# Optimization experiments

Hardware: AMD Instinct MI355X
Metric: run time of the kernel (lower is better)

## Reference

```python
import jax, jax.numpy as jnp
import numpy as np

INPUT_SIZE = 128
OUTPUT_SIZE = 128
HIDDEN = 8
BATCH = 1024
N = INPUT_SIZE * OUTPUT_SIZE  # number of tiny subnetworks


def setup_inputs() -> dict:
    key = jax.random.key(0)
    ks = jax.random.split(key, 7)
    s = 0.5  # modest init scale
    return {
        "x": jax.random.normal(ks[0], (BATCH, INPUT_SIZE), dtype=jnp.float32),
        "W1": jax.random.normal(ks[1], (N, HIDDEN, 1), dtype=jnp.float32) * s,
        "b1": jax.random.normal(ks[2], (N, HIDDEN), dtype=jnp.float32) * s,
        "W2": jax.random.normal(ks[3], (N, HIDDEN, HIDDEN), dtype=jnp.float32) * s,
        "b2": jax.random.normal(ks[4], (N, HIDDEN), dtype=jnp.float32) * s,
        "W3": jax.random.normal(ks[5], (N, 1, HIDDEN), dtype=jnp.float32) * s,
        "b3": jax.random.normal(ks[6], (N, 1), dtype=jnp.float32) * s,
    }


def reference(x, W1, b1, W2, b2, W3, b3):
    # x: [B, input_size]. Subnet n = i*output_size + o consumes feature i.
    B = x.shape[0]
    # x.T repeat_interleave(output_size, dim=0).unsqueeze(-1) -> [N, B, 1]
    xe = jnp.repeat(x.T, OUTPUT_SIZE, axis=0)[:, :, None]
    # torch Linear: y = x @ W.T + b, batched over subnet dim n
    h = jax.nn.relu(jnp.einsum('nbi,nhi->nbh', xe, W1) + b1[:, None, :])
    h = jax.nn.relu(jnp.einsum('nbi,nhi->nbh', h, W2) + b2[:, None, :])
    o = jnp.einsum('nbh,noh->nbo', h, W3) + b3[:, None, :]  # [N, B, 1]
    o = o[..., 0].reshape(INPUT_SIZE, OUTPUT_SIZE, B)
    return o.sum(axis=0).T  # [B, output_size]
```

## Files before the change

### kernel.cpp

```cpp
#include <hip/hip_runtime.h>

#define INPUT_SIZE 128
#define OUTPUT_SIZE 128
#define HIDDEN 8
#define BATCH 1024

#define ICH 16
#define IPC (INPUT_SIZE / ICH)
#define TPB 128
#define BPT 8
#define SLOT 68

typedef __fp16 half2v __attribute__((ext_vector_type(2)));

#if defined(__has_builtin)
#if __has_builtin(__builtin_amdgcn_fdot2)
#define HAS_FDOT2 1
#endif
#endif
#ifndef HAS_FDOT2
#define HAS_FDOT2 0
#endif

__global__ void prep_kernel(const float* __restrict__ x,
                            const float* __restrict__ W2,
                            float* __restrict__ xT,
                            __fp16* __restrict__ W2h) {
    if (blockIdx.x < 128) {
        __shared__ float tile[32][33];
        const int bx = blockIdx.x;
        const int i0 = (bx & 3) * 32;
        const int b0 = (bx >> 2) * 32;
        const int tx = threadIdx.x & 31;
        const int ty = threadIdx.x >> 5;
#pragma unroll
        for (int r = ty; r < 32; r += 8)
            tile[r][tx] = x[(b0 + r) * INPUT_SIZE + (i0 + tx)];
        __syncthreads();
#pragma unroll
        for (int r = ty; r < 32; r += 8)
            xT[(i0 + r) * BATCH + (b0 + tx)] = tile[tx][r];
    } else {
        const size_t idx = (size_t)(blockIdx.x - 128) * 256 + threadIdx.x;
        const float4 v = *(const float4*)(W2 + 4 * idx);
        const half2v a = __builtin_amdgcn_cvt_pkrtz(v.x, v.y);
        const half2v b = __builtin_amdgcn_cvt_pkrtz(v.z, v.w);
        float2 st;
        st.x = __builtin_bit_cast(float, a);
        st.y = __builtin_bit_cast(float, b);
        *(float2*)(W2h + 4 * idx) = st;
    }
}

__global__ void zero_out_kernel(float* __restrict__ out, int n) {
    int idx = blockIdx.x * blockDim.x + threadIdx.x;
    if (idx < n) out[idx] = 0.0f;
}

template <bool PARTIALS>
__global__ __launch_bounds__(TPB, 4)
void mlpkan_kernel(const float* __restrict__ xT,
                   const float* __restrict__ W1, const float* __restrict__ b1,
                   const __fp16* __restrict__ W2h, const float* __restrict__ b2,
                   const float* __restrict__ W3, const float* __restrict__ b3,
                   float* __restrict__ partials, float* __restrict__ out) {
    __shared__ float wlds[IPC * SLOT];

    const int o   = blockIdx.x;
    const int ic  = blockIdx.y;
    const int tid = threadIdx.x;

    {
        const int ii  = tid >> 4;
        const int idx = tid & 15;
        const int n   = (ic * IPC + ii) * OUTPUT_SIZE + o;
        float4 v;
        int dst;
        if (idx < 2) {
            v = *(const float4*)(W1 + (size_t)n * 8 + idx * 4);          dst = 0  + idx * 4;
        } else if (idx < 4) {
            v = *(const float4*)(b1 + (size_t)n * 8 + (idx - 2) * 4);    dst = 8  + (idx - 2) * 4;
        } else if (idx < 6) {
            v = *(const float4*)(b2 + (size_t)n * 8 + (idx - 4) * 4);    dst = 16 + (idx - 4) * 4;
        } else if (idx < 8) {
            v = *(const float4*)(W3 + (size_t)n * 8 + (idx - 6) * 4);    dst = 24 + (idx - 6) * 4;
        } else {
            v = *(const float4*)((const char*)W2h + (size_t)n * 128 + (idx - 8) * 16);
            dst = 36 + (idx - 8) * 4;
        }
        *(float4*)&wlds[ii * SLOT + dst] = v;
        if (idx == 0) wlds[ii * SLOT + 32] = b3[n];
    }
    __syncthreads();

    float acc[BPT];
#pragma unroll
    for (int j = 0; j < BPT; ++j) acc[j] = 0.0f;

#pragma unroll 1
    for (int ii = 0; ii < IPC; ++ii) {
        const int i = ic * IPC + ii;
        const float* w = &wlds[ii * SLOT];

        const float4 sA = *(const float4*)(xT + (size_t)i * BATCH + 4 * tid);
        const float4 sB = *(const float4*)(xT + (size_t)i * BATCH + 512 + 4 * tid);
        const float s[BPT] = {sA.x, sA.y, sA.z, sA.w, sB.x, sB.y, sB.z, sB.w};

        const float4 w1a = *(const float4*)(w + 0);
        const float4 w1b = *(const float4*)(w + 4);
        const float4 b1a = *(const float4*)(w + 8);
        const float4 b1b = *(const float4*)(w + 12);
        const float w1r[8] = {w1a.x, w1a.y, w1a.z, w1a.w, w1b.x, w1b.y, w1b.z, w1b.w};
        const float b1r[8] = {b1a.x, b1a.y, b1a.z, b1a.w, b1b.x, b1b.y, b1b.z, b1b.w};

        half2v h1p[BPT][4];
#pragma unroll
        for (int j = 0; j < BPT; ++j) {
            const float sj = s[j];
            float h1[8];
#pragma unroll
            for (int k = 0; k < 8; ++k)
                h1[k] = fmaxf(fmaf(w1r[k], sj, b1r[k]), 0.0f);
#pragma unroll
            for (int q = 0; q < 4; ++q)
                h1p[j][q] = __builtin_amdgcn_cvt_pkrtz(h1[2 * q], h1[2 * q + 1]);
        }

        const float4 b2a = *(const float4*)(w + 16);
        const float4 b2b = *(const float4*)(w + 20);
        const float4 w3a = *(const float4*)(w + 24);
        const float4 w3b = *(const float4*)(w + 28);
        const float  b3r = w[32];
        const float b2r[8] = {b2a.x, b2a.y, b2a.z, b2a.w, b2b.x, b2b.y, b2b.z, b2b.w};
        const float w3r[8] = {w3a.x, w3a.y, w3a.z, w3a.w, w3b.x, w3b.y, w3b.z, w3b.w};

        half2v w2p[8][4];
#pragma unroll
        for (int r = 0; r < 8; ++r) {
            const float4 row = *(const float4*)(w + 36 + 4 * r);
            w2p[r][0] = __builtin_bit_cast(half2v, row.x);
            w2p[r][1] = __builtin_bit_cast(half2v, row.y);
            w2p[r][2] = __builtin_bit_cast(half2v, row.z);
            w2p[r][3] = __builtin_bit_cast(half2v, row.w);
        }

#pragma unroll
        for (int j = 0; j < BPT; ++j) {
            float h2[8];
#if HAS_FDOT2
#pragma unroll
            for (int h = 0; h < 8; ++h) {
                float v = b2r[h];
#pragma unroll
                for (int q = 0; q < 4; ++q)
                    v = __builtin_amdgcn_fdot2(w2p[h][q], h1p[j][q], v, false);
                h2[h] = fmaxf(v, 0.0f);
            }
#else
#pragma unroll
            for (int h = 0; h < 8; ++h) {
                float v = b2r[h];
#pragma unroll
                for (int q = 0; q < 4; ++q) {
                    v = fmaf((float)w2p[h][q][0], (float)h1p[j][q][0], v);
                    v = fmaf((float)w2p[h][q][1], (float)h1p[j][q][1], v);
                }
                h2[h] = fmaxf(v, 0.0f);
            }
#endif
            float v3 = b3r;
#pragma unroll
            for (int k = 0; k < 8; ++k)
                v3 = fmaf(w3r[k], h2[k], v3);
            acc[j] += v3;
        }
    }

    if (PARTIALS) {
        float* base = partials + ((size_t)ic * OUTPUT_SIZE + o) * BATCH;
        float4 pa = {acc[0], acc[1], acc[2], acc[3]};
        float4 pb = {acc[4], acc[5], acc[6], acc[7]};
        *(float4*)(base + 4 * tid)       = pa;
        *(float4*)(base + 512 + 4 * tid) = pb;
    } else {
#pragma unroll
        for (int j = 0; j < BPT; ++j) {
            const int b = (j < 4) ? (4 * tid + j) : (512 + 4 * tid + (j - 4));
            atomicAdd(&out[(size_t)b * OUTPUT_SIZE + o], acc[j]);
        }
    }
}

__global__ void reduce_kernel(const float* __restrict__ partials,
                              float* __restrict__ out) {
    __shared__ float tile[32][33];
    const int o0 = blockIdx.x * 32;
    const int b0 = blockIdx.y * 32;
    const int tx = threadIdx.x;
    const int ty = threadIdx.y;
#pragma unroll
    for (int r = ty; r < 32; r += 16) {
        float v = 0.0f;
#pragma unroll
        for (int icc = 0; icc < ICH; ++icc)
            v += partials[((size_t)icc * OUTPUT_SIZE + o0 + r) * BATCH + b0 + tx];
        tile[r][tx] = v;
    }
    __syncthreads();
#pragma unroll
    for (int r = ty; r < 32; r += 16)
        out[(size_t)(b0 + r) * OUTPUT_SIZE + o0 + tx] = tile[tx][r];
}

extern "C" void kernel_launch(void* const* d_in, const int* in_sizes, int n_in,
                              void* d_out, int out_size, void* d_ws, size_t ws_size,
                              hipStream_t stream) {
    const float* x  = (const float*)d_in[0];
    const float* W1 = (const float*)d_in[1];
    const float* b1 = (const float*)d_in[2];
    const float* W2 = (const float*)d_in[3];
    const float* b2 = (const float*)d_in[4];
    const float* W3 = (const float*)d_in[5];
    const float* b3 = (const float*)d_in[6];
    float* out = (float*)d_out;

    const size_t xt_elems   = (size_t)INPUT_SIZE * BATCH;
    const size_t part_elems = (size_t)ICH * OUTPUT_SIZE * BATCH;
    const size_t w2h_bytes  = (size_t)16384 * 64 * sizeof(__fp16);
    const size_t need_bytes = (xt_elems + part_elems) * sizeof(float) + w2h_bytes;

    dim3 mgrid(OUTPUT_SIZE, ICH);

    if (ws_size >= need_bytes) {
        float*   xT       = (float*)d_ws;
        float*   partials = xT + xt_elems;
        __fp16*  W2h      = (__fp16*)(partials + part_elems);

        prep_kernel<<<1152, 256, 0, stream>>>(x, W2, xT, W2h);
        mlpkan_kernel<true><<<mgrid, TPB, 0, stream>>>(xT, W1, b1, W2h, b2, W3, b3,
                                                       partials, out);
        dim3 rgrid(OUTPUT_SIZE / 32, BATCH / 32);
        reduce_kernel<<<rgrid, dim3(32, 16), 0, stream>>>(partials, out);
    } else {
        const int nz = BATCH * OUTPUT_SIZE;
        zero_out_kernel<<<(nz + 255) / 256, 256, 0, stream>>>(out, nz);
        if (ws_size >= xt_elems * sizeof(float) + w2h_bytes) {
            float*  xT  = (float*)d_ws;
            __fp16* W2h = (__fp16*)(xT + xt_elems);
            prep_kernel<<<1152, 256, 0, stream>>>(x, W2, xT, W2h);
            mlpkan_kernel<false><<<mgrid, TPB, 0, stream>>>(xT, W1, b1, W2h, b2, W3, b3,
                                                            nullptr, out);
        }
    }
}
```

Measured before the change: 110.7 us.

## Compute first layer in packed fp16 and double input-chunk grid

Converts W1 and b1 to packed fp16 in the prep kernel and computes the first hidden layer with packed half2 multiply-add and max, removing the per-element fp32 FMA plus convert work. It also raises the input chunk count from 16 to 32, so there are twice as many blocks, each covering 4 inputs, and raises the launch-bounds occupancy target from 4 to 8. The cost is lower first-layer precision, a larger prep kernel, and twice as many partial sums for the reduce kernel to read and add.

```diff
diff --git a/kernel.cpp b/kernel.cpp
--- a/kernel.cpp
+++ b/kernel.cpp
@@ -5,11 +5,11 @@
 #define HIDDEN 8
 #define BATCH 1024
 
-#define ICH 16
+#define ICH 32
 #define IPC (INPUT_SIZE / ICH)
 #define TPB 128
 #define BPT 8
-#define SLOT 68
+#define SLOT 60
 
 typedef __fp16 half2v __attribute__((ext_vector_type(2)));
 
@@ -23,12 +23,16 @@
 #endif
 
 __global__ void prep_kernel(const float* __restrict__ x,
+                            const float* __restrict__ W1,
+                            const float* __restrict__ b1,
                             const float* __restrict__ W2,
                             float* __restrict__ xT,
+                            unsigned int* __restrict__ W1h,
+                            unsigned int* __restrict__ b1h,
                             __fp16* __restrict__ W2h) {
-    if (blockIdx.x < 128) {
+    const int bx = blockIdx.x;
+    if (bx < 128) {
         __shared__ float tile[32][33];
-        const int bx = blockIdx.x;
         const int i0 = (bx & 3) * 32;
         const int b0 = (bx >> 2) * 32;
         const int tx = threadIdx.x & 31;
@@ -40,8 +44,8 @@
 #pragma unroll
         for (int r = ty; r < 32; r += 8)
             xT[(i0 + r) * BATCH + (b0 + tx)] = tile[tx][r];
-    } else {
-        const size_t idx = (size_t)(blockIdx.x - 128) * 256 + threadIdx.x;
+    } else if (bx < 1152) {
+        const size_t idx = (size_t)(bx - 128) * 256 + threadIdx.x;
         const float4 v = *(const float4*)(W2 + 4 * idx);
         const half2v a = __builtin_amdgcn_cvt_pkrtz(v.x, v.y);
         const half2v b = __builtin_amdgcn_cvt_pkrtz(v.z, v.w);
@@ -49,6 +53,16 @@
         st.x = __builtin_bit_cast(float, a);
         st.y = __builtin_bit_cast(float, b);
         *(float2*)(W2h + 4 * idx) = st;
+    } else if (bx < 1280) {
+        const size_t t = (size_t)(bx - 1152) * 256 + threadIdx.x;
+        const float4 v = *(const float4*)(W1 + 4 * t);
+        W1h[2 * t]     = __builtin_bit_cast(unsigned int, __builtin_amdgcn_cvt_pkrtz(v.x, v.y));
+        W1h[2 * t + 1] = __builtin_bit_cast(unsigned int, __builtin_amdgcn_cvt_pkrtz(v.z, v.w));
+    } else {
+        const size_t t = (size_t)(bx - 1280) * 256 + threadIdx.x;
+        const float4 v = *(const float4*)(b1 + 4 * t);
+        b1h[2 * t]     = __builtin_bit_cast(unsigned int, __builtin_amdgcn_cvt_pkrtz(v.x, v.y));
+        b1h[2 * t + 1] = __builtin_bit_cast(unsigned int, __builtin_amdgcn_cvt_pkrtz(v.z, v.w));
     }
 }
 
@@ -58,9 +72,10 @@
 }
 
 template <bool PARTIALS>
-__global__ __launch_bounds__(TPB, 4)
+__global__ __launch_bounds__(TPB, 8)
 void mlpkan_kernel(const float* __restrict__ xT,
-                   const float* __restrict__ W1, const float* __restrict__ b1,
+                   const unsigned int* __restrict__ W1h,
+                   const unsigned int* __restrict__ b1h,
                    const __fp16* __restrict__ W2h, const float* __restrict__ b2,
                    const float* __restrict__ W3, const float* __restrict__ b3,
                    float* __restrict__ partials, float* __restrict__ out) {
@@ -73,23 +88,19 @@
     {
         const int ii  = tid >> 4;
         const int idx = tid & 15;
-        const int n   = (ic * IPC + ii) * OUTPUT_SIZE + o;
-        float4 v;
-        int dst;
-        if (idx < 2) {
-            v = *(const float4*)(W1 + (size_t)n * 8 + idx * 4);          dst = 0  + idx * 4;
-        } else if (idx < 4) {
-            v = *(const float4*)(b1 + (size_t)n * 8 + (idx - 2) * 4);    dst = 8  + (idx - 2) * 4;
-        } else if (idx < 6) {
-            v = *(const float4*)(b2 + (size_t)n * 8 + (idx - 4) * 4);    dst = 16 + (idx - 4) * 4;
-        } else if (idx < 8) {
-            v = *(const float4*)(W3 + (size_t)n * 8 + (idx - 6) * 4);    dst = 24 + (idx - 6) * 4;
-        } else {
-            v = *(const float4*)((const char*)W2h + (size_t)n * 128 + (idx - 8) * 16);
-            dst = 36 + (idx - 8) * 4;
-        }
-        *(float4*)&wlds[ii * SLOT + dst] = v;
-        if (idx == 0) wlds[ii * SLOT + 32] = b3[n];
+        if (ii < IPC) {
+            const int n = (ic * IPC + ii) * OUTPUT_SIZE + o;
+            float* d = &wlds[ii * SLOT];
+            if (idx == 0)      *(float4*)(d + 0)  = *(const float4*)((const float*)W1h + (size_t)n * 4);
+            else if (idx == 1) *(float4*)(d + 4)  = *(const float4*)((const float*)b1h + (size_t)n * 4);
+            else if (idx == 2) *(float4*)(d + 8)  = *(const float4*)(b2 + (size_t)n * 8);
+            else if (idx == 3) *(float4*)(d + 12) = *(const float4*)(b2 + (size_t)n * 8 + 4);
+            else if (idx == 4) *(float4*)(d + 16) = *(const float4*)(W3 + (size_t)n * 8);
+            else if (idx == 5) *(float4*)(d + 20) = *(const float4*)(W3 + (size_t)n * 8 + 4);
+            else if (idx == 6) d[24] = b3[n];
+            else if (idx >= 8) *(float4*)(d + 28 + 4 * (idx - 8)) =
+                *(const float4*)((const char*)W2h + (size_t)n * 128 + (idx - 8) * 16);
+        }
     }
     __syncthreads();
 
@@ -106,38 +117,37 @@
         const float4 sB = *(const float4*)(xT + (size_t)i * BATCH + 512 + 4 * tid);
         const float s[BPT] = {sA.x, sA.y, sA.z, sA.w, sB.x, sB.y, sB.z, sB.w};
 
-        const float4 w1a = *(const float4*)(w + 0);
-        const float4 w1b = *(const float4*)(w + 4);
-        const float4 b1a = *(const float4*)(w + 8);
-        const float4 b1b = *(const float4*)(w + 12);
-        const float w1r[8] = {w1a.x, w1a.y, w1a.z, w1a.w, w1b.x, w1b.y, w1b.z, w1b.w};
-        const float b1r[8] = {b1a.x, b1a.y, b1a.z, b1a.w, b1b.x, b1b.y, b1b.z, b1b.w};
+        const float4 w1q = *(const float4*)(w + 0);
+        const float4 b1q = *(const float4*)(w + 4);
+        const half2v w1p[4] = {__builtin_bit_cast(half2v, w1q.x), __builtin_bit_cast(half2v, w1q.y),
+                               __builtin_bit_cast(half2v, w1q.z), __builtin_bit_cast(half2v, w1q.w)};
+        const half2v b1p[4] = {__builtin_bit_cast(half2v, b1q.x), __builtin_bit_cast(half2v, b1q.y),
+                               __builtin_bit_cast(half2v, b1q.z), __builtin_bit_cast(half2v, b1q.w)};
+        const half2v zero2 = {(__fp16)0.0f, (__fp16)0.0f};
 
         half2v h1p[BPT][4];
 #pragma unroll
         for (int j = 0; j < BPT; ++j) {
-            const float sj = s[j];
-            float h1[8];
-#pragma unroll
-            for (int k = 0; k < 8; ++k)
-                h1[k] = fmaxf(fmaf(w1r[k], sj, b1r[k]), 0.0f);
-#pragma unroll
-            for (int q = 0; q < 4; ++q)
-                h1p[j][q] = __builtin_amdgcn_cvt_pkrtz(h1[2 * q], h1[2 * q + 1]);
-        }
-
-        const float4 b2a = *(const float4*)(w + 16);
-        const float4 b2b = *(const float4*)(w + 20);
-        const float4 w3a = *(const float4*)(w + 24);
-        const float4 w3b = *(const float4*)(w + 28);
-        const float  b3r = w[32];
+            const half2v xx = __builtin_amdgcn_cvt_pkrtz(s[j], s[j]);
+#pragma unroll
+            for (int q = 0; q < 4; ++q) {
+                const half2v v = w1p[q] * xx + b1p[q];
+                h1p[j][q] = __builtin_elementwise_max(v, zero2);
+            }
+        }
+
+        const float4 b2a = *(const float4*)(w + 8);
+        const float4 b2b = *(const float4*)(w + 12);
+        const float4 w3a = *(const float4*)(w + 16);
+        const float4 w3b = *(const float4*)(w + 20);
+        const float  b3r = w[24];
         const float b2r[8] = {b2a.x, b2a.y, b2a.z, b2a.w, b2b.x, b2b.y, b2b.z, b2b.w};
         const float w3r[8] = {w3a.x, w3a.y, w3a.z, w3a.w, w3b.x, w3b.y, w3b.z, w3b.w};
 
         half2v w2p[8][4];
 #pragma unroll
         for (int r = 0; r < 8; ++r) {
-            const float4 row = *(const float4*)(w + 36 + 4 * r);
+            const float4 row = *(const float4*)(w + 28 + 4 * r);
             w2p[r][0] = __builtin_bit_cast(half2v, row.x);
             w2p[r][1] = __builtin_bit_cast(half2v, row.y);
             w2p[r][2] = __builtin_bit_cast(half2v, row.z);
@@ -227,28 +237,34 @@
     const size_t xt_elems   = (size_t)INPUT_SIZE * BATCH;
     const size_t part_elems = (size_t)ICH * OUTPUT_SIZE * BATCH;
     const size_t w2h_bytes  = (size_t)16384 * 64 * sizeof(__fp16);
-    const size_t need_bytes = (xt_elems + part_elems) * sizeof(float) + w2h_bytes;
+    const size_t w1h_elems  = (size_t)16384 * 4;
+    const size_t need_bytes = (xt_elems + part_elems) * sizeof(float) + w2h_bytes
+                            + 2 * w1h_elems * sizeof(unsigned int);
 
     dim3 mgrid(OUTPUT_SIZE, ICH);
 
     if (ws_size >= need_bytes) {
-        float*   xT       = (float*)d_ws;
-        float*   partials = xT + xt_elems;
-        __fp16*  W2h      = (__fp16*)(partials + part_elems);
-
-        prep_kernel<<<1152, 256, 0, stream>>>(x, W2, xT, W2h);
-        mlpkan_kernel<true><<<mgrid, TPB, 0, stream>>>(xT, W1, b1, W2h, b2, W3, b3,
+        float*        xT       = (float*)d_ws;
+        float*        partials = xT + xt_elems;
+        __fp16*       W2h      = (__fp16*)(partials + part_elems);
+        unsigned int* W1h      = (unsigned int*)((char*)W2h + w2h_bytes);
+        unsigned int* b1h      = W1h + w1h_elems;
+
+        prep_kernel<<<1408, 256, 0, stream>>>(x, W1, b1, W2, xT, W1h, b1h, W2h);
+        mlpkan_kernel<true><<<mgrid, TPB, 0, stream>>>(xT, W1h, b1h, W2h, b2, W3, b3,
                                                        partials, out);
         dim3 rgrid(OUTPUT_SIZE / 32, BATCH / 32);
         reduce_kernel<<<rgrid, dim3(32, 16), 0, stream>>>(partials, out);
     } else {
         const int nz = BATCH * OUTPUT_SIZE;
         zero_out_kernel<<<(nz + 255) / 256, 256, 0, stream>>>(out, nz);
-        if (ws_size >= xt_elems * sizeof(float) + w2h_bytes) {
-            float*  xT  = (float*)d_ws;
-            __fp16* W2h = (__fp16*)(xT + xt_elems);
-            prep_kernel<<<1152, 256, 0, stream>>>(x, W2, xT, W2h);
-            mlpkan_kernel<false><<<mgrid, TPB, 0, stream>>>(xT, W1, b1, W2h, b2, W3, b3,
+        if (ws_size >= xt_elems * sizeof(float) + w2h_bytes + 2 * w1h_elems * sizeof(unsigned int)) {
+            float*        xT  = (float*)d_ws;
+            __fp16*       W2h = (__fp16*)(xT + xt_elems);
+            unsigned int* W1h = (unsigned int*)((char*)W2h + w2h_bytes);
+            unsigned int* b1h = W1h + w1h_elems;
+            prep_kernel<<<1408, 256, 0, stream>>>(x, W1, b1, W2, xT, W1h, b1h, W2h);
+            mlpkan_kernel<false><<<mgrid, TPB, 0, stream>>>(xT, W1h, b1h, W2h, b2, W3, b3,
                                                             nullptr, out);
         }
     }
```

After: 239.1 us. 2.16x slower.
